# Kernel optimization log

Measured on AMD Instinct MI355X. Metric: run time of the kernel, lower is better.

The kernel has to match this reference:

```python
import jax, jax.numpy as jnp
import numpy as np

B_, L_, DM = 8, 1024, 256
DS, DC, EX = 16, 4, 2
DI = EX * DM            # d_inner = 512
DTR = max(1, DM // 16)  # dt_rank = 16


def setup_inputs() -> dict:
    key = jax.random.key(0)
    ks = iter(jax.random.split(key, 40))
    def n(shape, s=0.02):
        return jax.random.normal(next(ks), shape, jnp.float32) * s
    inp = {"x": jax.random.normal(next(ks), (B_, L_, DM), jnp.float32)}
    inp["norm_g"] = jnp.ones((DM,), jnp.float32)
    inp["norm_b"] = jnp.zeros((DM,), jnp.float32)
    for m in ("f", "b"):
        inp[f"inW_{m}"] = n((DM, 2 * DI))
        inp[f"convW_{m}"] = n((DI, DC))
        inp[f"convB_{m}"] = jnp.zeros((DI,), jnp.float32)
        inp[f"xW_{m}"] = n((DI, DTR + 2 * DS))
        inp[f"dtW_{m}"] = n((DTR, DI))
        inp[f"dtB_{m}"] = jnp.zeros((DI,), jnp.float32)
        # ALog init: log of [1..dState] repeated over dInner rows
        inp[f"ALog_{m}"] = jnp.log(jnp.tile(jnp.arange(1, DS + 1, dtype=jnp.float32), (DI, 1)))
        inp[f"Dp_{m}"] = jnp.ones((DI,), jnp.float32)
        inp[f"outW_{m}"] = n((DI, DM))
    inp["fusW"] = n((2 * DM, DM))
    inp["fusB"] = jnp.zeros((DM,), jnp.float32)
    return inp


def _dw_conv(x, w, b):
    # causal depthwise conv1d: x [B,L,DI], w [DI,DC] -> [B,L,DI]
    xc = jnp.transpose(x, (0, 2, 1))  # B,DI,L
    out = jax.lax.conv_general_dilated(
        xc, w[:, None, :], window_strides=(1,), padding=[(DC - 1, 0)],
        dimension_numbers=("NCH", "OIH", "NCH"), feature_group_count=DI)
    return jnp.transpose(out + b[:, None], (0, 2, 1))


def _ssm(x, xW, dtW, dtB, ALog, Dp):
    # x: [B,L,DI]
    A = -jnp.exp(ALog)                                   # [DI,DS]
    xdbl = x @ xW                                        # [B,L,DTR+2*DS]
    dlt, Bp, Cp = jnp.split(xdbl, [DTR, DTR + DS], axis=-1)
    delta = jax.nn.softplus(dlt @ dtW + dtB)             # [B,L,DI]
    dA = jnp.exp(delta[..., None] * A)                   # [B,L,DI,DS]
    dBx = (delta * x)[..., None] * Bp[:, :, None, :]     # [B,L,DI,DS]

    def step(h, t):
        a, bb, c = t
        h = a * h + bb                                   # [B,DI,DS]
        y = jnp.einsum('bdn,bn->bd', h, c)
        return h, y

    h0 = jnp.zeros((x.shape[0], DI, DS), x.dtype)
    _, ys = jax.lax.scan(step, h0, (jnp.moveaxis(dA, 1, 0),
                                    jnp.moveaxis(dBx, 1, 0),
                                    jnp.moveaxis(Cp, 1, 0)))
    return jnp.moveaxis(ys, 0, 1) + Dp * x               # [B,L,DI]


def _mamba(x, inW, convW, convB, xW, dtW, dtB, ALog, Dp, outW):
    xr = x @ inW                                         # [B,L,2*DI]
    xs, res = jnp.split(xr, 2, axis=-1)
    xs = jax.nn.silu(_dw_conv(xs, convW, convB))
    y = _ssm(xs, xW, dtW, dtB, ALog, Dp)
    return (y * jax.nn.silu(res)) @ outW                 # [B,L,DM]


def reference(x, norm_g, norm_b,
              inW_f, convW_f, convB_f, xW_f, dtW_f, dtB_f, ALog_f, Dp_f, outW_f,
              inW_b, convW_b, convB_b, xW_b, dtW_b, dtB_b, ALog_b, Dp_b, outW_b,
              fusW, fusB):
    # LayerNorm
    mu = x.mean(-1, keepdims=True)
    var = ((x - mu) ** 2).mean(-1, keepdims=True)
    xn = (x - mu) * jax.lax.rsqrt(var + 1e-5) * norm_g + norm_b
    # forward-direction Mamba
    xf = _mamba(xn, inW_f, convW_f, convB_f, xW_f, dtW_f, dtB_f, ALog_f, Dp_f, outW_f)
    # backward-direction Mamba (flip along time)
    xb = _mamba(jnp.flip(xn, 1), inW_b, convW_b, convB_b, xW_b, dtW_b, dtB_b, ALog_b, Dp_b, outW_b)
    xb = jnp.flip(xb, 1)
    fused = jnp.concatenate([xf, xb], axis=-1) @ fusW + fusB
    return x + fused  # dropout is identity in eval
```

## Files before the change

kernel.cpp:

```cpp
#include <hip/hip_runtime.h>
#include <cmath>

typedef __bf16 bf16x8 __attribute__((ext_vector_type(8)));
typedef __bf16 bf16x4 __attribute__((ext_vector_type(4)));
typedef float  f32x4  __attribute__((ext_vector_type(4)));
typedef float  f32x2  __attribute__((ext_vector_type(2)));

#define B_  8
#define L_  1024
#define DM  256
#define DI  512
#define DS  16
#define DTR 16
#define M_  (B_*L_)
#define NC  64
#define CT  16

__device__ inline float softplus_f(float z){
  return (z > 20.f) ? z : __logf(1.f + __expf(z));
}
__device__ inline float silu_f(float z){
  return z / (1.f + __expf(-z));
}

__device__ inline int flag_from_x(const void* x){
  const unsigned short* u = (const unsigned short*)x;
  int lane = threadIdx.x & 63;
  unsigned short v = u[2*lane];
  int e = (v >> 7) & 0xFF;
  unsigned long long m = __ballot(e >= 160 || e < 96);
  return __popcll(m) > 16;
}

struct PrepJob { const void* src; void* dst; int rows; int cols; int f32out; };
struct PrepArgs { PrepJob j[26]; int nj; };

__global__ __launch_bounds__(256) void prep_k(PrepArgs a, const void* xsrc){
  const int f = flag_from_x(xsrc);
  int e = blockIdx.x*256 + threadIdx.x;
  #pragma unroll 1
  for (int jj=0; jj<a.nj; jj++){
    int sz = a.j[jj].rows * a.j[jj].cols;
    if (e < sz){
      int cols = a.j[jj].cols;
      int r = e / cols, c = e - r*cols;
      float v = f ? ((const float*)a.j[jj].src)[e] : (float)((const __bf16*)a.j[jj].src)[e];
      if (a.j[jj].f32out) ((float*)a.j[jj].dst)[c*a.j[jj].rows + r] = v;
      else ((__bf16*)a.j[jj].dst)[(long)c*a.j[jj].rows + r] = (__bf16)v;
      return;
    }
    e -= sz;
  }
}

__global__ __launch_bounds__(256) void lnw_k(
    const void* x, const __bf16* g, const __bf16* bb, __bf16* xn,
    const __bf16* fusWt, const __bf16* outWr0, const __bf16* outWr1,
    __bf16* BtC0, __bf16* BtC1)
{
  const int bx = blockIdx.x;
  const int tid = threadIdx.x;
  const int lane = tid & 63;
  const int wid = tid >> 6;

  if (bx < M_/4){
    const int f = flag_from_x(x);
    long row = (long)bx*4 + wid;
    long base = row*DM + lane*4;
    float v0,v1,v2,v3;
    if (f){ f32x4 xv = *(const f32x4*)((const float*)x + base);
            v0=xv[0]; v1=xv[1]; v2=xv[2]; v3=xv[3]; }
    else  { bf16x4 xv = *(const bf16x4*)((const __bf16*)x + base);
            v0=(float)xv[0]; v1=(float)xv[1]; v2=(float)xv[2]; v3=(float)xv[3]; }
    float s = v0+v1+v2+v3;
    float q = v0*v0+v1*v1+v2*v2+v3*v3;
    #pragma unroll
    for (int off=32; off>0; off>>=1){ s += __shfl_xor(s,off); q += __shfl_xor(q,off); }
    float mu = s*(1.f/DM), var = q*(1.f/DM)-mu*mu;
    float rs = rsqrtf(var+1e-5f);
    bf16x4 gv = *(const bf16x4*)(g + lane*4);
    bf16x4 bv = *(const bf16x4*)(bb + lane*4);
    bf16x4 o;
    o[0]=(__bf16)((v0-mu)*rs*(float)gv[0]+(float)bv[0]);
    o[1]=(__bf16)((v1-mu)*rs*(float)gv[1]+(float)bv[1]);
    o[2]=(__bf16)((v2-mu)*rs*(float)gv[2]+(float)bv[2]);
    o[3]=(__bf16)((v3-mu)*rs*(float)gv[3]+(float)bv[3]);
    *(bf16x4*)(xn + base) = o;
  } else {
    int b2 = bx - M_/4;
    int wz  = b2 >> 5;
    int rem = b2 & 31;
    int gx = rem & 3, gy = rem >> 2;
    const __bf16* A  = fusWt + wz*DM;
    const __bf16* Bt = wz ? outWr1 : outWr0;
    __bf16* C = wz ? BtC1 : BtC0;
    const int mBase = (gx*4 + wid)*16;
    const int nBase = gy*64;
    const int lm = lane & 15;
    const int kq = (lane >> 4)*8;
    long aoff = (long)(mBase+lm)*(2*DM) + kq;
    long boff[4];
    #pragma unroll
    for (int j=0;j<4;j++) boff[j] = (long)(nBase+j*16+lm)*DM + kq;
    f32x4 acc[4] = {};
    #pragma unroll
    for (int k0=0;k0<DM;k0+=32){
      bf16x8 af = *(const bf16x8*)(A + aoff + k0);
      bf16x8 bfr[4];
      #pragma unroll
      for (int j=0;j<4;j++) bfr[j] = *(const bf16x8*)(Bt + boff[j] + k0);
      #pragma unroll
      for (int j=0;j<4;j++)
        acc[j] = __builtin_amdgcn_mfma_f32_16x16x32_bf16(af, bfr[j], acc[j], 0,0,0);
    }
    #pragma unroll
    for (int rr=0;rr<4;rr++){
      int r = mBase + (lane>>4)*4 + rr;
      #pragma unroll
      for (int j=0;j<4;j++){
        int c = nBase + j*16 + lm;
        C[(long)r*DI + c] = (__bf16)acc[j][rr];
      }
    }
  }
}

template<int BM,int BN,int KK>
__global__ __launch_bounds__(256) void gemm_in_k(
    const __bf16* A, const __bf16* B0, const __bf16* B1,
    __bf16* xz0, __bf16* xz1, __bf16* res0, __bf16* res1,
    int lda, int ldb)
{
  constexpr int TM = BM/2, TN = BN/2;
  constexpr int WMT = TM/16, WNT = TN/16;
  constexpr int LA = BM/64, LB = BN/64;

  const int dir = blockIdx.z;
  const __bf16* Bt = dir ? B1 : B0;
  __bf16* xz  = dir ? xz1 : xz0;
  __bf16* res = dir ? res1 : res0;
  const int tid  = threadIdx.x;
  const int lane = tid & 63;
  const int wid  = tid >> 6;
  const int wm = wid & 1;
  const int wn = wid >> 1;
  const int mBase = blockIdx.x * BM;
  const int nBase = blockIdx.y * BN;
  const int lm = lane & 15;
  const int kq = (lane >> 4) * 8;

  __shared__ __bf16 As[BM*32];
  __shared__ __bf16 Bs[BN*32];

  const __bf16* aS[LA];
  const __bf16* bS[LB];
  {
    int colk = (tid & 3) * 8;
    #pragma unroll
    for (int ld=0; ld<LA; ld++){
      int r = mBase + ld*64 + (tid >> 2);
      if (dir==1){ int b = r >> 10, t = r & (L_-1); r = (b<<10) + (L_-1-t); }
      aS[ld] = A + (long)r*lda + colk;
    }
    #pragma unroll
    for (int ld=0; ld<LB; ld++){
      int r = nBase + ld*64 + (tid >> 2);
      bS[ld] = Bt + (long)r*ldb + colk;
    }
  }

  f32x4 acc[WMT][WNT] = {};
  for (int k0=0; k0<KK; k0+=32){
    #pragma unroll
    for (int ld=0; ld<LA; ld++)
      __builtin_amdgcn_global_load_lds(
        (const __attribute__((address_space(1))) void*)(aS[ld] + k0),
        (__attribute__((address_space(3))) void*)(&As[ld*2048 + tid*8]), 16, 0, 0);
    #pragma unroll
    for (int ld=0; ld<LB; ld++)
      __builtin_amdgcn_global_load_lds(
        (const __attribute__((address_space(1))) void*)(bS[ld] + k0),
        (__attribute__((address_space(3))) void*)(&Bs[ld*2048 + tid*8]), 16, 0, 0);
    __syncthreads();
    bf16x8 af[WMT], bfr[WNT];
    #pragma unroll
    for (int i=0;i<WMT;i++) af[i]  = *(const bf16x8*)&As[(wm*TM + i*16 + lm)*32 + kq];
    #pragma unroll
    for (int j=0;j<WNT;j++) bfr[j] = *(const bf16x8*)&Bs[(wn*TN + j*16 + lm)*32 + kq];
    #pragma unroll
    for (int i=0;i<WMT;i++)
      #pragma unroll
      for (int j=0;j<WNT;j++)
        acc[i][j] = __builtin_amdgcn_mfma_f32_16x16x32_bf16(af[i], bfr[j], acc[i][j], 0,0,0);
    __syncthreads();
  }

  #pragma unroll
  for (int i=0;i<WMT;i++){
    #pragma unroll
    for (int rr=0;rr<4;rr++){
      int r = mBase + wm*TM + i*16 + (lane>>4)*4 + rr;
      #pragma unroll
      for (int j=0;j<WNT;j++){
        int c = nBase + wn*TN + j*16 + lm;
        float v = acc[i][j][rr];
        if (c < DI) xz[(long)r*DI + c] = (__bf16)v;
        else        res[(long)r*DI + (c-DI)] = (__bf16)v;
      }
    }
  }
}

template<int BM,int BN,int KK>
__global__ __launch_bounds__(256) void gemm_fin_k(
    const __bf16* Af, const __bf16* Ab,
    const __bf16* Bt0, const __bf16* Bt1,
    void* Cout, const __bf16* bias, const void* resid)
{
  constexpr int TM = BM/2, TN = BN/2;
  constexpr int WMT = TM/16, WNT = TN/16;
  constexpr int LA = BM/64, LB = BN/64;

  const int of = flag_from_x(resid);
  const int tid  = threadIdx.x;
  const int lane = tid & 63;
  const int wid  = tid >> 6;
  const int wm = wid & 1;
  const int wn = wid >> 1;
  const int mBase = blockIdx.x * BM;
  const int nBase = blockIdx.y * BN;
  const int lm = lane & 15;
  const int kq = (lane >> 4) * 8;

  __shared__ __bf16 As[BM*32];
  __shared__ __bf16 Bs[BN*32];

  f32x4 acc[WMT][WNT] = {};
  #pragma unroll 1
  for (int dd=0; dd<2; dd++){
    const __bf16* A  = dd ? Ab  : Af;
    const __bf16* Bt = dd ? Bt1 : Bt0;
    const __bf16* aS[LA];
    const __bf16* bS[LB];
    {
      int colk = (tid & 3) * 8;
      #pragma unroll
      for (int ld=0; ld<LA; ld++){
        int r = mBase + ld*64 + (tid >> 2);
        if (dd==1){ int b = r >> 10, t = r & (L_-1); r = (b<<10) + (L_-1-t); }
        aS[ld] = A + (long)r*DI + colk;
      }
      #pragma unroll
      for (int ld=0; ld<LB; ld++){
        int r = nBase + ld*64 + (tid >> 2);
        bS[ld] = Bt + (long)r*DI + colk;
      }
    }
    for (int k0=0; k0<KK; k0+=32){
      #pragma unroll
      for (int ld=0; ld<LA; ld++)
        __builtin_amdgcn_global_load_lds(
          (const __attribute__((address_space(1))) void*)(aS[ld] + k0),
          (__attribute__((address_space(3))) void*)(&As[ld*2048 + tid*8]), 16, 0, 0);
      #pragma unroll
      for (int ld=0; ld<LB; ld++)
        __builtin_amdgcn_global_load_lds(
          (const __attribute__((address_space(1))) void*)(bS[ld] + k0),
          (__attribute__((address_space(3))) void*)(&Bs[ld*2048 + tid*8]), 16, 0, 0);
      __syncthreads();
      bf16x8 af[WMT], bfr[WNT];
      #pragma unroll
      for (int i=0;i<WMT;i++) af[i]  = *(const bf16x8*)&As[(wm*TM + i*16 + lm)*32 + kq];
      #pragma unroll
      for (int j=0;j<WNT;j++) bfr[j] = *(const bf16x8*)&Bs[(wn*TN + j*16 + lm)*32 + kq];
      #pragma unroll
      for (int i=0;i<WMT;i++)
        #pragma unroll
        for (int j=0;j<WNT;j++)
          acc[i][j] = __builtin_amdgcn_mfma_f32_16x16x32_bf16(af[i], bfr[j], acc[i][j], 0,0,0);
      __syncthreads();
    }
  }

  #pragma unroll
  for (int i=0;i<WMT;i++){
    #pragma unroll
    for (int rr=0;rr<4;rr++){
      int r = mBase + wm*TM + i*16 + (lane>>4)*4 + rr;
      #pragma unroll
      for (int j=0;j<WNT;j++){
        int c = nBase + wn*TN + j*16 + lm;
        float v = acc[i][j][rr];
        float rsd = of ? ((const float*)resid)[(long)r*DM + c]
                       : (float)((const __bf16*)resid)[(long)r*DM + c];
        v += (float)bias[c] + rsd;
        if (of) ((float*)Cout)[(long)r*DM + c] = v;
        else    ((__bf16*)Cout)[(long)r*DM + c] = (__bf16)v;
      }
    }
  }
}

template<int WMT,int WNT,int BWM,int BWN,int KK>
__global__ __launch_bounds__(64*BWM*BWN) void gemm_r_k(
    const __bf16* A0, const __bf16* A1,
    const __bf16* B0, const __bf16* B1,
    float* C0, float* C1,
    int lda, int ldb, int ldc)
{
  const int dir = blockIdx.z;
  const __bf16* A  = dir ? A1 : A0;
  const __bf16* Bt = dir ? B1 : B0;
  float* C = dir ? C1 : C0;
  const int tid  = threadIdx.x;
  const int lane = tid & 63;
  const int wid  = tid >> 6;
  const int wm = wid % BWM;
  const int wn = wid / BWM;
  const int mBase = (blockIdx.x*BWM + wm) * (WMT*16);
  const int nBase = (blockIdx.y*BWN + wn) * (WNT*16);
  const int lm = lane & 15;
  const int kq = (lane >> 4) * 8;

  long aoff[WMT];
  #pragma unroll
  for (int i=0;i<WMT;i++) aoff[i] = (long)(mBase + i*16 + lm) * lda + kq;
  long boff[WNT];
  #pragma unroll
  for (int j=0;j<WNT;j++) boff[j] = (long)(nBase + j*16 + lm) * ldb + kq;

  f32x4 acc[WMT][WNT] = {};
  #pragma unroll
  for (int k0=0; k0<KK; k0+=32){
    bf16x8 af[WMT], bfr[WNT];
    #pragma unroll
    for (int i=0;i<WMT;i++) af[i]  = *(const bf16x8*)(A  + aoff[i] + k0);
    #pragma unroll
    for (int j=0;j<WNT;j++) bfr[j] = *(const bf16x8*)(Bt + boff[j] + k0);
    #pragma unroll
    for (int i=0;i<WMT;i++)
      #pragma unroll
      for (int j=0;j<WNT;j++)
        acc[i][j] = __builtin_amdgcn_mfma_f32_16x16x32_bf16(af[i], bfr[j], acc[i][j], 0,0,0);
  }

  #pragma unroll
  for (int i=0;i<WMT;i++)
    #pragma unroll
    for (int rr=0;rr<4;rr++){
      int r = mBase + i*16 + (lane>>4)*4 + rr;
      #pragma unroll
      for (int j=0;j<WNT;j++){
        int c = nBase + j*16 + lm;
        C[(long)r*ldc + c] = acc[i][j][rr];
      }
    }
}

__global__ __launch_bounds__(256) void conv_k(
    const __bf16* xz0, const __bf16* xz1,
    const float* cw0, const float* cw1,
    const __bf16* cb0, const __bf16* cb1,
    __bf16* xs0, __bf16* xs1)
{
  const int dir = blockIdx.z;
  const __bf16* xz = dir ? xz1 : xz0;
  const float*  cw = dir ? cw1 : cw0;
  const __bf16* cb = dir ? cb1 : cb0;
  __bf16* xs = dir ? xs1 : xs0;

  int gid = blockIdx.x*256 + threadIdx.x;
  int c8 = gid & 63;
  int t  = (gid >> 6) & (L_-1);
  int b  = gid >> 16;
  int cbase = c8*8;

  float acc[8];
  bf16x8 bb = *(const bf16x8*)(cb + cbase);
  #pragma unroll
  for (int c=0;c<8;c++) acc[c] = (float)bb[c];
  #pragma unroll
  for (int j=0;j<4;j++){
    int tj = t - 3 + j;
    if (tj >= 0){
      bf16x8 xv = *(const bf16x8*)(xz + ((long)(b*L_ + tj))*DI + cbase);
      #pragma unroll
      for (int c=0;c<8;c++) acc[c] += (float)xv[c] * cw[j*DI + cbase + c];
    }
  }
  bf16x8 outv;
  #pragma unroll
  for (int c=0;c<8;c++) outv[c] = (__bf16)silu_f(acc[c]);
  *(bf16x8*)(xs + ((long)(b*L_ + t))*DI + cbase) = outv;
}

__global__ __launch_bounds__(256) void scanA_k(
    const float* xd0, const float* xd1,
    const __bf16* xs0, const __bf16* xs1,
    const float* dw0, const float* dw1,
    const __bf16* dtB0, const __bf16* dtB1,
    const float* ALf0, const float* ALf1,
    float* hend, float* sumd)
{
  const int dir = blockIdx.z;
  const float*  xd  = dir ? xd1 : xd0;
  const __bf16* xs  = dir ? xs1 : xs0;
  const float*  dw  = dir ? dw1 : dw0;
  const __bf16* dtB = dir ? dtB1 : dtB0;
  const float*  ALf = dir ? ALf1 : ALf0;

  const int b   = blockIdx.y;
  const int c   = blockIdx.x >> 1;
  const int dg_ = blockIdx.x & 1;
  const int tid = threadIdx.x;
  const int d   = dg_*256 + tid;
  const int db  = dir*8 + b;
  const long row0 = (long)b*L_ + c*CT;

  __shared__ float sAB[CT][32];
  if (tid < CT*8){ int e = tid*4; int t = e>>5, cc = e&31;
    *(f32x4*)&sAB[t][cc] = *(const f32x4*)(xd + (row0+t)*48 + cc); }

  f32x2 dw2[8];
  { const f32x4* p = (const f32x4*)(dw + d*DTR);
    #pragma unroll
    for (int q=0;q<4;q++){ f32x4 v=p[q];
      dw2[q*2]   = f32x2{v[0],v[1]};
      dw2[q*2+1] = f32x2{v[2],v[3]}; } }
  float A[16];
  { const f32x4* p = (const f32x4*)(ALf + d*DS);
    #pragma unroll
    for (int q=0;q<4;q++){ f32x4 v=p[q];
      A[q*4]=-__expf(v[0]); A[q*4+1]=-__expf(v[1]); A[q*4+2]=-__expf(v[2]); A[q*4+3]=-__expf(v[3]); } }
  bool pow_ok = true;
  #pragma unroll
  for (int n=0;n<16;n++) pow_ok = pow_ok && (fabsf(A[n] + (float)(n+1)) < 0.003f*(n+1));
  const float dtbv = (float)dtB[d];

  f32x2 h2[8];
  #pragma unroll
  for (int i=0;i<8;i++) h2[i] = f32x2{0.f,0.f};
  float sdelta = 0.f;
  __syncthreads();

  if (pow_ok){
    #pragma unroll 2
    for (int t=0;t<CT;t++){
      f32x2 z2 = f32x2{dtbv, 0.f};
      #pragma unroll
      for (int i=0;i<8;i++){
        f32x2 qv = *(const f32x2*)&sAB[t][i*2];
        z2 += qv*dw2[i];
      }
      float delta = softplus_f(z2[0]+z2[1]);
      sdelta += delta;
      float xv = (float)xs[(row0+t)*DI + d];
      float dx = delta*xv;
      f32x2 dx2 = f32x2{dx, dx};
      float e1 = __expf(-delta), e2v = e1*e1;
      f32x2 e22 = f32x2{e2v, e2v};
      f32x2 pw = f32x2{e1, e2v};
      #pragma unroll
      for (int i=0;i<8;i++){
        f32x2 Bv = *(const f32x2*)&sAB[t][16+i*2];
        h2[i] = pw*h2[i] + dx2*Bv;
        pw = pw*e22;
      }
    }
  } else {
    #pragma unroll 2
    for (int t=0;t<CT;t++){
      f32x2 z2 = f32x2{dtbv, 0.f};
      #pragma unroll
      for (int i=0;i<8;i++){
        f32x2 qv = *(const f32x2*)&sAB[t][i*2];
        z2 += qv*dw2[i];
      }
      float delta = softplus_f(z2[0]+z2[1]);
      sdelta += delta;
      float xv = (float)xs[(row0+t)*DI + d];
      float dx = delta*xv;
      #pragma unroll
      for (int i=0;i<8;i++){
        f32x2 Bv = *(const f32x2*)&sAB[t][16+i*2];
        f32x2 pw = f32x2{__expf(delta*A[i*2]), __expf(delta*A[i*2+1])};
        h2[i] = pw*h2[i] + f32x2{dx,dx}*Bv;
      }
    }
  }

  long hb = (((long)db*NC + c)*DI + d)*16;
  f32x4* hp = (f32x4*)(hend + hb);
  #pragma unroll
  for (int q=0;q<4;q++){
    f32x4 v; v[0]=h2[q*2][0]; v[1]=h2[q*2][1]; v[2]=h2[q*2+1][0]; v[3]=h2[q*2+1][1];
    hp[q]=v;
  }
  sumd[((long)db*NC + c)*DI + d] = sdelta;
}

__global__ __launch_bounds__(256) void scanB_k(
    const float* ALf0, const float* ALf1,
    const float* hend, const float* sumd, float* Hbuf)
{
  int gid = blockIdx.x*256 + threadIdx.x;
  int n  = gid & 15;
  int d  = (gid>>4) & 511;
  int db = gid >> 13;
  const float* ALf = (db>=8) ? ALf1 : ALf0;
  float A_dn = -__expf(ALf[d*DS + n]);
  float H = 0.f;
  #pragma unroll 1
  for (int c=0;c<NC;c++){
    long base = (((long)db*NC + c)*DI + d)*16 + n;
    Hbuf[base] = H;
    float S = sumd[((long)db*NC + c)*DI + d];
    H = hend[base] + __expf(A_dn*S)*H;
  }
}

__global__ __launch_bounds__(256) void scanC_k(
    const float* xd0, const float* xd1,
    const __bf16* xs0, const __bf16* xs1,
    __bf16* res0, __bf16* res1,
    const float* dw0, const float* dw1,
    const __bf16* dtB0, const __bf16* dtB1,
    const float* ALf0, const float* ALf1,
    const __bf16* Dp0, const __bf16* Dp1,
    const float* Hbuf)
{
  const int dir = blockIdx.z;
  const float*  xd  = dir ? xd1 : xd0;
  const __bf16* xs  = dir ? xs1 : xs0;
  __bf16*       res = dir ? res1 : res0;
  const float*  dw  = dir ? dw1 : dw0;
  const __bf16* dtB = dir ? dtB1 : dtB0;
  const float*  ALf = dir ? ALf1 : ALf0;
  const __bf16* Dp  = dir ? Dp1 : Dp0;

  const int b   = blockIdx.y;
  const int c   = blockIdx.x >> 1;
  const int dg_ = blockIdx.x & 1;
  const int tid = threadIdx.x;
  const int d   = dg_*256 + tid;
  const int db  = dir*8 + b;
  const long row0 = (long)b*L_ + c*CT;

  __shared__ float sX[CT][48];
  if (tid < CT*12){ int e = tid*4; int t = e/48, cc = e - t*48;
    *(f32x4*)&sX[t][cc] = *(const f32x4*)(xd + (row0+t)*48 + cc); }

  f32x2 dw2[8];
  { const f32x4* p = (const f32x4*)(dw + d*DTR);
    #pragma unroll
    for (int q=0;q<4;q++){ f32x4 v=p[q];
      dw2[q*2]   = f32x2{v[0],v[1]};
      dw2[q*2+1] = f32x2{v[2],v[3]}; } }
  float A[16];
  { const f32x4* p = (const f32x4*)(ALf + d*DS);
    #pragma unroll
    for (int q=0;q<4;q++){ f32x4 v=p[q];
      A[q*4]=-__expf(v[0]); A[q*4+1]=-__expf(v[1]); A[q*4+2]=-__expf(v[2]); A[q*4+3]=-__expf(v[3]); } }
  bool pow_ok = true;
  #pragma unroll
  for (int n=0;n<16;n++) pow_ok = pow_ok && (fabsf(A[n] + (float)(n+1)) < 0.003f*(n+1));
  const float dtbv = (float)dtB[d];

  f32x2 h2[8];
  { long hb = (((long)db*NC + c)*DI + d)*16;
    const f32x4* p = (const f32x4*)(Hbuf + hb);
    #pragma unroll
    for (int q=0;q<4;q++){ f32x4 v = p[q];
      h2[q*2]   = f32x2{v[0],v[1]};
      h2[q*2+1] = f32x2{v[2],v[3]}; } }
  const float Dpv = (float)Dp[d];
  __syncthreads();

  if (pow_ok){
    #pragma unroll 2
    for (int t=0;t<CT;t++){
      long row = row0 + t;
      f32x2 z2 = f32x2{dtbv, 0.f};
      #pragma unroll
      for (int i=0;i<8;i++){
        f32x2 qv = *(const f32x2*)&sX[t][i*2];
        z2 += qv*dw2[i];
      }
      float delta = softplus_f(z2[0]+z2[1]);
      float xv = (float)xs[row*DI + d];
      float dx = delta*xv;
      f32x2 dx2 = f32x2{dx, dx};
      float e1 = __expf(-delta), e2v = e1*e1;
      f32x2 e22 = f32x2{e2v, e2v};
      f32x2 pw = f32x2{e1, e2v};
      f32x2 p2 = f32x2{0.f, 0.f};
      #pragma unroll
      for (int i=0;i<8;i++){
        f32x2 Bv = *(const f32x2*)&sX[t][16+i*2];
        f32x2 Cv = *(const f32x2*)&sX[t][32+i*2];
        h2[i] = pw*h2[i] + dx2*Bv;
        p2 += h2[i]*Cv;
        pw = pw*e22;
      }
      float yv = p2[0] + p2[1] + Dpv*xv;
      float rv = (float)res[row*DI + d];
      res[row*DI + d] = (__bf16)(yv * silu_f(rv));
    }
  } else {
    #pragma unroll 2
    for (int t=0;t<CT;t++){
      long row = row0 + t;
      f32x2 z2 = f32x2{dtbv, 0.f};
      #pragma unroll
      for (int i=0;i<8;i++){
        f32x2 qv = *(const f32x2*)&sX[t][i*2];
        z2 += qv*dw2[i];
      }
      float delta = softplus_f(z2[0]+z2[1]);
      float xv = (float)xs[row*DI + d];
      float dx = delta*xv;
      f32x2 p2 = f32x2{0.f, 0.f};
      #pragma unroll
      for (int i=0;i<8;i++){
        f32x2 Bv = *(const f32x2*)&sX[t][16+i*2];
        f32x2 Cv = *(const f32x2*)&sX[t][32+i*2];
        f32x2 pw = f32x2{__expf(delta*A[i*2]), __expf(delta*A[i*2+1])};
        h2[i] = pw*h2[i] + f32x2{dx,dx}*Bv;
        p2 += h2[i]*Cv;
      }
      float yv = p2[0] + p2[1] + Dpv*xv;
      float rv = (float)res[row*DI + d];
      res[row*DI + d] = (__bf16)(yv * silu_f(rv));
    }
  }
}

extern "C" void kernel_launch(void* const* d_in, const int* in_sizes, int n_in,
                              void* d_out, int out_size, void* d_ws, size_t ws_size,
                              hipStream_t stream)
{
  const size_t MB = 1u<<20;
  if (ws_size < 160*MB) return;

  char* w = (char*)d_ws;
  __bf16* xz[2]  = {(__bf16*)(w + 0),      (__bf16*)(w + 8*MB)};
  __bf16* res[2] = {(__bf16*)(w + 16*MB),  (__bf16*)(w + 24*MB)};
  __bf16* xsc[2] = {(__bf16*)(w + 32*MB),  (__bf16*)(w + 40*MB)};
  __bf16* xn     = (__bf16*)(w + 48*MB);
  float*  xdbl[2]= {(float*)(w + 58*MB),   (float*)(w + 58*MB + (size_t)M_*48*4)};

  char* wp = w + 52*MB;
  auto carve = [&](size_t bytes)->void*{
    void* p = wp;
    wp += (bytes + 255) & ~(size_t)255;
    return p;
  };
  __bf16 *inWt[2], *xWt[2], *outWr[2], *BtC[2];
  float *dtWt[2], *convWt[2];
  for (int m=0;m<2;m++){
    inWt[m]   = (__bf16*)carve((size_t)(2*DI)*DM*2);
    xWt[m]    = (__bf16*)carve((size_t)48*DI*2);
    outWr[m]  = (__bf16*)carve((size_t)DI*DM*2);
    BtC[m]    = (__bf16*)carve((size_t)DM*DI*2);
    dtWt[m]   = (float*)carve((size_t)DI*DTR*4);
    convWt[m] = (float*)carve((size_t)4*DI*4);
  }
  __bf16* fusWt = (__bf16*)carve((size_t)DM*(2*DM)*2);
  float* ALf[2] = {(float*)carve((size_t)DI*DS*4), (float*)carve((size_t)DI*DS*4)};

  char* cp = w + 57*MB;
  auto carve2 = [&](size_t elems)->__bf16*{
    __bf16* p = (__bf16*)cp;
    cp += (elems*2 + 255) & ~(size_t)255;
    return p;
  };
  __bf16* ngc = carve2(DM);
  __bf16* nbc = carve2(DM);
  __bf16 *convBc[2], *dtBc[2], *Dpc[2];
  for (int m=0;m<2;m++){
    convBc[m] = carve2(DI);
    dtBc[m]   = carve2(DI);
    Dpc[m]    = carve2(DI);
  }
  __bf16* fusBc = carve2(DM);

  float* hend = (float*)(w + 90*MB);
  float* sumd = (float*)(w + 124*MB);
  float* Hbuf = (float*)(w + 127*MB);

  PrepArgs pa;
  int ji = 0;
  size_t tot = 0;
  auto addj = [&](const void* s, void* dst, int rows, int cols, int f32o){
    pa.j[ji++] = {s, dst, rows, cols, f32o};
    tot += (size_t)rows*cols;
  };
  for (int m=0;m<2;m++){
    int base = 3 + m*9;
    addj(d_in[base+0], inWt[m],  DM,  2*DI, 0);
    addj(d_in[base+3], xWt[m],   DI,  48,   0);
    addj(d_in[base+8], outWr[m], 1,   DI*DM,0);
    addj(d_in[base+4], dtWt[m],  DTR, DI,   1);
    addj(d_in[base+1], convWt[m],DI,  4,    1);
    addj(d_in[base+2], convBc[m],1, DI, 0);
    addj(d_in[base+5], dtBc[m],  1, DI, 0);
    addj(d_in[base+6], (void*)ALf[m], 1, DI*DS, 1);
    addj(d_in[base+7], Dpc[m],   1, DI, 0);
  }
  addj(d_in[21], fusWt, 2*DM, DM, 0);
  addj(d_in[1],  ngc, 1, DM, 0);
  addj(d_in[2],  nbc, 1, DM, 0);
  addj(d_in[22], fusBc, 1, DM, 0);
  pa.nj = ji;
  prep_k<<<(int)((tot+255)/256), 256, 0, stream>>>(pa, d_in[0]);

  lnw_k<<<M_/4 + 64, 256, 0, stream>>>(
      d_in[0], ngc, nbc, xn, fusWt, outWr[0], outWr[1], BtC[0], BtC[1]);

  gemm_in_k<128,128,256><<<dim3(M_/128, (2*DI)/128, 2), 256, 0, stream>>>(
      xn, inWt[0], inWt[1], xz[0], xz[1], res[0], res[1], DM, DM);
  conv_k<<<dim3((M_*64)/256, 1, 2), 256, 0, stream>>>(
      xz[0], xz[1], convWt[0], convWt[1], convBc[0], convBc[1], xsc[0], xsc[1]);
  gemm_r_k<1,3,4,1,DI><<<dim3(M_/64, 1, 2), 256, 0, stream>>>(
      xsc[0], xsc[1], xWt[0], xWt[1], xdbl[0], xdbl[1], DI, DI, 48);

  scanA_k<<<dim3(NC*2, B_, 2), 256, 0, stream>>>(
      xdbl[0], xdbl[1], xsc[0], xsc[1], dtWt[0], dtWt[1],
      dtBc[0], dtBc[1], ALf[0], ALf[1], hend, sumd);
  scanB_k<<<131072/256, 256, 0, stream>>>(ALf[0], ALf[1], hend, sumd, Hbuf);
  scanC_k<<<dim3(NC*2, B_, 2), 256, 0, stream>>>(
      xdbl[0], xdbl[1], xsc[0], xsc[1], res[0], res[1],
      dtWt[0], dtWt[1], dtBc[0], dtBc[1], ALf[0], ALf[1], Dpc[0], Dpc[1], Hbuf);

  gemm_fin_k<64,64,DI><<<dim3(M_/64, DM/64, 1), 256, 0, stream>>>(
      res[0], res[1], BtC[0], BtC[1], d_out, fusBc, d_in[0]);
}
```

Baseline: 254.8 us.

## Use larger scan chunks and tiled shared-memory transposes for big weights

The chunked scan now uses 32 chunks of 32 timesteps instead of 64 of 16. This halves the number of chunk-boundary states that the inter-chunk pass (scanB) must combine, at the cost of longer sequential work per thread and fewer blocks. The large weight transposes (inW for both directions and fusW) move from the element-wise prep kernel, which did strided uncoalesced writes, to a new 64x64 shared-memory tiled transpose kernel with coalesced reads and writes. This adds one extra kernel launch.

Result: no change. 251.6 us (-1.2%).

```diff
diff --git a/kernel.cpp b/kernel.cpp
--- a/kernel.cpp
+++ b/kernel.cpp
@@ -13,8 +13,8 @@
 #define DS  16
 #define DTR 16
 #define M_  (B_*L_)
-#define NC  64
-#define CT  16
+#define NC  32
+#define CT  32
 
 __device__ inline float softplus_f(float z){
   return (z > 20.f) ? z : __logf(1.f + __expf(z));
@@ -50,6 +50,36 @@
       return;
     }
     e -= sz;
+  }
+}
+
+struct TJob { const void* src; __bf16* dst; int R; int C; };
+struct TArgs { TJob j[3]; int ntiles[3]; int nj; };
+
+__global__ __launch_bounds__(256) void tpose_k(TArgs a, const void* xsrc){
+  const int f = flag_from_x(xsrc);
+  __shared__ float tile[64][65];
+  int bid = blockIdx.x;
+  int jj = 0;
+  while (jj < a.nj-1 && bid >= a.ntiles[jj]) { bid -= a.ntiles[jj]; jj++; }
+  const TJob J = a.j[jj];
+  const int tpr = J.C >> 6;
+  const int tr = bid / tpr, tc = bid - tr*tpr;
+  const int r0 = tr*64, c0 = tc*64;
+  const int tid = threadIdx.x;
+  #pragma unroll
+  for (int i=0;i<16;i++){
+    int idx = i*256 + tid;
+    int r = idx >> 6, c = idx & 63;
+    long off = (long)(r0+r)*J.C + c0 + c;
+    tile[r][c] = f ? ((const float*)J.src)[off] : (float)((const __bf16*)J.src)[off];
+  }
+  __syncthreads();
+  #pragma unroll
+  for (int i=0;i<16;i++){
+    int idx = i*256 + tid;
+    int c = idx >> 6, r = idx & 63;
+    J.dst[(long)(c0+c)*J.R + r0 + r] = (__bf16)tile[r][c];
   }
 }
 
@@ -418,7 +448,7 @@
   const long row0 = (long)b*L_ + c*CT;
 
   __shared__ float sAB[CT][32];
-  if (tid < CT*8){ int e = tid*4; int t = e>>5, cc = e&31;
+  { int e = tid*4; int t = e>>5, cc = e&31;
     *(f32x4*)&sAB[t][cc] = *(const f32x4*)(xd + (row0+t)*48 + cc); }
 
   f32x2 dw2[8];
@@ -547,7 +577,7 @@
   const long row0 = (long)b*L_ + c*CT;
 
   __shared__ float sX[CT][48];
-  if (tid < CT*12){ int e = tid*4; int t = e/48, cc = e - t*48;
+  for (int v=tid; v<CT*12; v+=256){ int e = v*4; int t = e/48, cc = e - t*48;
     *(f32x4*)&sX[t][cc] = *(const f32x4*)(xd + (row0+t)*48 + cc); }
 
   f32x2 dw2[8];
@@ -697,7 +727,6 @@
   };
   for (int m=0;m<2;m++){
     int base = 3 + m*9;
-    addj(d_in[base+0], inWt[m],  DM,  2*DI, 0);
     addj(d_in[base+3], xWt[m],   DI,  48,   0);
     addj(d_in[base+8], outWr[m], 1,   DI*DM,0);
     addj(d_in[base+4], dtWt[m],  DTR, DI,   1);
@@ -707,12 +736,18 @@
     addj(d_in[base+6], (void*)ALf[m], 1, DI*DS, 1);
     addj(d_in[base+7], Dpc[m],   1, DI, 0);
   }
-  addj(d_in[21], fusWt, 2*DM, DM, 0);
   addj(d_in[1],  ngc, 1, DM, 0);
   addj(d_in[2],  nbc, 1, DM, 0);
   addj(d_in[22], fusBc, 1, DM, 0);
   pa.nj = ji;
   prep_k<<<(int)((tot+255)/256), 256, 0, stream>>>(pa, d_in[0]);
+
+  TArgs ta;
+  ta.j[0] = { d_in[3],  inWt[0], DM,   2*DI }; ta.ntiles[0] = (DM/64)*((2*DI)/64);
+  ta.j[1] = { d_in[12], inWt[1], DM,   2*DI }; ta.ntiles[1] = (DM/64)*((2*DI)/64);
+  ta.j[2] = { d_in[21], fusWt,   2*DM, DM   }; ta.ntiles[2] = ((2*DM)/64)*(DM/64);
+  ta.nj = 3;
+  tpose_k<<<ta.ntiles[0]+ta.ntiles[1]+ta.ntiles[2], 256, 0, stream>>>(ta, d_in[0]);
 
   lnw_k<<<M_/4 + 64, 256, 0, stream>>>(
       d_in[0], ngc, nbc, xn, fusWt, outWr[0], outWr[1], BtC[0], BtC[1]);
```
